# Kernel tuning notes

Hardware: AMD Instinct MI355X
Metric: run time of the kernel (lower is better)

The kernel has to match this reference:

```python
import jax, jax.numpy as jnp
import numpy as np

B, C, T = 16, 129, 2000
NF, ED, K = 40, 64, 16

def setup_inputs() -> dict:
    key = jax.random.key(0)
    ks = iter(jax.random.split(key, 48))
    def n(shape, s=0.05):
        return jax.random.normal(next(ks), shape, jnp.float32) * s
    inp = {
        'x': jax.random.normal(next(ks), (B, C, T), jnp.float32),
        # temporal conv (1,25) pad (0,12) + BN (inference running stats)
        'tconv_w': n((NF, 1, 1, 25)), 'tconv_b': jnp.zeros((NF,)),
        'tbn_g': jnp.ones((NF,)), 'tbn_b': jnp.zeros((NF,)), 'tbn_m': n((NF,)), 'tbn_v': jnp.ones((NF,)),
        # spatial conv (C,1) + BN
        'sconv_w': n((NF, NF, C, 1)), 'sconv_b': jnp.zeros((NF,)),
        'sbn_g': jnp.ones((NF,)), 'sbn_b': jnp.zeros((NF,)), 'sbn_m': n((NF,)), 'sbn_v': jnp.ones((NF,)),
        # separable: depthwise (1,15) pad (0,7), pointwise 1x1 -> 2*NF, BN
        'dw_w': n((NF, 1, 1, 15)), 'dw_b': jnp.zeros((NF,)),
        'pw_w': n((2 * NF, NF, 1, 1)), 'pw_b': jnp.zeros((2 * NF,)),
        'pbn_g': jnp.ones((2 * NF,)), 'pbn_b': jnp.zeros((2 * NF,)), 'pbn_m': n((2 * NF,)), 'pbn_v': jnp.ones((2 * NF,)),
        # projection 2*NF -> ED
        'proj_w': n((ED, 2 * NF)), 'proj_b': jnp.zeros((ED,)),
        # ENN cell 0 (input ED)
        'wx0': n((K, ED)), 'L0': jnp.eye(K, dtype=jnp.float32) + 0.1 * n((K, K), 1.0),
        'll0': jnp.asarray(np.log(0.1), jnp.float32), 'b0': jnp.zeros((K,)),
        'ln0_g': jnp.ones((K,)), 'ln0_b': jnp.zeros((K,)),
        # ENN cell 1 (input K)
        'wx1': n((K, K)), 'L1': jnp.eye(K, dtype=jnp.float32) + 0.1 * n((K, K), 1.0),
        'll1': jnp.asarray(np.log(0.1), jnp.float32), 'b1': jnp.zeros((K,)),
        'ln1_g': jnp.ones((K,)), 'ln1_b': jnp.zeros((K,)),
        # collapse
        'wq_w': n((K, K)), 'wq_b': jnp.zeros((K,)), 'log_temp': jnp.asarray(0.0, jnp.float32),
    }
    return inp

def _conv(x, w, b, pad, groups=1):
    y = jax.lax.conv_general_dilated(
        x, w, window_strides=(1, 1), padding=pad,
        dimension_numbers=('NCHW', 'OIHW', 'NCHW'), feature_group_count=groups)
    return y + b[None, :, None, None]

def _bn(x, g, b, m, v, eps=1e-5):
    inv = g / jnp.sqrt(v + eps)
    return x * inv[None, :, None, None] + (b - m * inv)[None, :, None, None]

def _cell(x, h, Wx, L, ll, b, g, be, eps=1e-5):
    E = L @ L.T  # PSD entanglement matrix [K,K]
    pre = x @ Wx.T + h @ E.T - jnp.exp(ll) * h + b
    mu = pre.mean(-1, keepdims=True)
    var = pre.var(-1, keepdims=True)
    pre = (pre - mu) / jnp.sqrt(var + eps) * g + be
    return jnp.tanh(pre)

def _forward(x, tconv_w, tconv_b, tbn_g, tbn_b, tbn_m, tbn_v,
             sconv_w, sconv_b, sbn_g, sbn_b, sbn_m, sbn_v,
             dw_w, dw_b, pw_w, pw_b, pbn_g, pbn_b, pbn_m, pbn_v,
             proj_w, proj_b,
             wx0, L0, ll0, b0, ln0_g, ln0_b,
             wx1, L1, ll1, b1, ln1_g, ln1_b,
             wq_w, wq_b, log_temp):
    # ---- SpatialCNN front-end (BN in inference mode, dropout=identity) ----
    o = x[:, None, :, :]                                        # [B,1,C,T]
    o = _conv(o, tconv_w, tconv_b, ((0, 0), (12, 12)))          # [B,NF,C,T]
    o = jax.nn.elu(_bn(o, tbn_g, tbn_b, tbn_m, tbn_v))
    o = _conv(o, sconv_w, sconv_b, ((0, 0), (0, 0)))            # [B,NF,1,T]
    o = jax.nn.elu(_bn(o, sbn_g, sbn_b, sbn_m, sbn_v))
    o = _conv(o, dw_w, dw_b, ((0, 0), (7, 7)), groups=NF)       # depthwise
    o = _conv(o, pw_w, pw_b, ((0, 0), (0, 0)))                  # [B,2NF,1,T]
    o = jax.nn.elu(_bn(o, pbn_g, pbn_b, pbn_m, pbn_v))
    Bn, Ch, _, Tt = o.shape
    o = o.reshape(Bn, Ch, Tt // 4, 4).mean(-1)                  # AvgPool (1,4) -> [B,2NF,T']
    feats = o.transpose(0, 2, 1) @ proj_w.T + proj_b            # [B,T',ED]
    # ---- Entangled RNN over T' steps (lax.scan) ----
    h_init = (jnp.zeros((Bn, K), feats.dtype), jnp.zeros((Bn, K), feats.dtype))
    def step(carry, xt):
        h0, h1 = carry
        h0 = _cell(xt, h0, wx0, L0, ll0, b0, ln0_g, ln0_b)
        h1 = _cell(h0, h1, wx1, L1, ll1, b1, ln1_g, ln1_b)
        return (h0, h1), None
    (h0, h1), _ = jax.lax.scan(step, h_init, feats.transpose(1, 0, 2))
    Z = h1                                                       # [B,K]
    # ---- Collapse attention ----
    q = Z @ wq_w.T + wq_b
    scores = jnp.sum(q * Z, axis=-1, keepdims=True)              # [B,1]
    alpha = jax.nn.softmax(scores / jnp.exp(log_temp), axis=-1)  # [B,1]
    return Z, alpha

def reference(x, tconv_w, tconv_b, tbn_g, tbn_b, tbn_m, tbn_v,
              sconv_w, sconv_b, sbn_g, sbn_b, sbn_m, sbn_v,
              dw_w, dw_b, pw_w, pw_b, pbn_g, pbn_b, pbn_m, pbn_v,
              proj_w, proj_b,
              wx0, L0, ll0, b0, ln0_g, ln0_b,
              wx1, L1, ll1, b1, ln1_g, ln1_b,
              wq_w, wq_b, log_temp):
    return _forward(x, tconv_w, tconv_b, tbn_g, tbn_b, tbn_m, tbn_v,
                    sconv_w, sconv_b, sbn_g, sbn_b, sbn_m, sbn_v,
                    dw_w, dw_b, pw_w, pw_b, pbn_g, pbn_b, pbn_m, pbn_v,
                    proj_w, proj_b,
                    wx0, L0, ll0, b0, ln0_g, ln0_b,
                    wx1, L1, ll1, b1, ln1_g, ln1_b,
                    wq_w, wq_b, log_temp)
```

## Files before the change

### kernel.cpp

```cpp
#include <hip/hip_runtime.h>
#include <math.h>

#define B_ 16
#define C_ 129
#define T_ 2000
#define NF_ 40
#define ED_ 64
#define K_ 16
#define TP_ 500

#define OFF_SB2 1040
#define OFF_PWC 1088
#define OFF_PB2 4288
#define OFF_WP  4368
#define OFF_BP  5648
#define OFF_M0  5664
#define OFF_M1  5920
#define OFF_W1A 6224
#define OFF_W2U 8192
#define OFF_XP  1495040
#define OFF_S2R 1623040

typedef __attribute__((ext_vector_type(8))) short s8v;
typedef __attribute__((ext_vector_type(4))) float f4v;

#define XROW 292

__device__ __forceinline__ float elu_f(float x) {
    return x > 0.f ? x : (__expf(x) - 1.f);
}
__device__ __forceinline__ float tanh2e_f(float a2) {
    return fmaf(-2.f,
                __builtin_amdgcn_rcpf(__builtin_amdgcn_exp2f(a2) + 1.f), 1.f);
}
__device__ __forceinline__ unsigned bfr(float v) {
    return (__float_as_uint(v) + 0x8000u) >> 16;
}

#define DPPF(v, ctrl) __int_as_float(__builtin_amdgcn_update_dpp( \
    0, __float_as_int(v), (ctrl), 0xF, 0xF, false))

#define RSUM16(s) do {                     \
    s += DPPF(s, 0x128);                   \
    s += DPPF(s, 0x124);                   \
    s += DPPF(s, 0x122);                   \
    s += DPPF(s, 0x121);                   \
} while (0)

#define RDLANE(v, L) __int_as_float(__builtin_amdgcn_readlane(__float_as_int(v), (L)))

#define C2F 2.8853900817779268f

struct P0 {
    const float *tconv_w, *tconv_b, *tbn_g, *tbn_b, *tbn_m, *tbn_v;
    const float *sconv_b, *sbn_g, *sbn_b, *sbn_m, *sbn_v;
    const float *pw_w, *pw_b, *pbn_g, *pbn_b, *pbn_m, *pbn_v;
    const float *proj_w, *proj_b, *wx0, *b0, *L0, *ll0, *L1, *ll1;
    const float *sconv_w;
    float* ws;
};

__global__ __launch_bounds__(256) void k0_all(P0 p) {
    const int tid = threadIdx.x;
    float* ws = p.ws;
    const float eps = 1e-5f;

    if (blockIdx.x < 1250) {
        const int i = blockIdx.x * 256 + tid;
        if (i < 320000)
            ((float4*)(ws + OFF_S2R))[i] = make_float4(0.f, 0.f, 0.f, 0.f);
        return;
    }
    if (blockIdx.x < 1444) {
        const int e = (blockIdx.x - 1250) * 256 + tid;
        if (e >= C_ * 3 * 2 * 64) return;
        unsigned short* w2b = (unsigned short*)(ws + OFF_W2U);
        const int c = e / 384;
        int r = e - c * 384;
        const int mt = r >> 7; r &= 127;
        const int kc = r >> 6;
        const int lane = r & 63;
        const int g = mt * 16 + (lane & 15);
        const float sinv = (g < NF_) ? p.sbn_g[g] * rsqrtf(p.sbn_v[g] + 1e-5f) : 0.f;
        unsigned short o[8];
#pragma unroll
        for (int j = 0; j < 8; ++j) {
            const int f = kc * 32 + (lane >> 4) * 8 + j;
            float v = 0.f;
            if (g < NF_ && f < NF_) v = p.sconv_w[g * (NF_ * C_) + f * C_ + c] * sinv;
            o[j] = (unsigned short)bfr(v);
        }
        unsigned short* dst = w2b + (size_t)e * 8;
#pragma unroll
        for (int j = 0; j < 8; ++j) dst[j] = o[j];
        return;
    }

    const int gtid = (blockIdx.x - 1444) * 256 + tid;
    const int stride = 8 * 256;
    for (int e = gtid; e < 192; e += stride) {
        const int mt = e >> 6, L = e & 63;
        const int f = mt * 16 + (L & 15);
        float inv = 0.f, bias = 0.f;
        if (f < NF_) {
            inv = p.tbn_g[f] / sqrtf(p.tbn_v[f] + eps);
            bias = p.tconv_b[f] * inv + p.tbn_b[f] - p.tbn_m[f] * inv;
        }
        unsigned short* dst = ((unsigned short*)(ws + OFF_W1A)) + e * 8;
#pragma unroll
        for (int j = 0; j < 8; ++j) {
            const int k = (L >> 4) * 8 + j;
            float v = 0.f;
            if (f < NF_) {
                if (k < 25) v = p.tconv_w[f * 25 + k] * inv;
                else if (k == 25) v = bias;
            }
            dst[j] = (unsigned short)bfr(v);
        }
    }
    for (int f = gtid; f < NF_; f += stride) {
        const float sinv = p.sbn_g[f] / sqrtf(p.sbn_v[f] + eps);
        ws[OFF_SB2 + f] = p.sconv_b[f] * sinv + p.sbn_b[f] - p.sbn_m[f] * sinv;
    }
    for (int e = gtid; e < 3200; e += stride) {
        const int g = e / 40;
        const float pinv = p.pbn_g[g] / sqrtf(p.pbn_v[g] + eps);
        ws[OFF_PWC + e] = p.pw_w[e] * pinv;
    }
    for (int g = gtid; g < 80; g += stride) {
        const float pinv = p.pbn_g[g] / sqrtf(p.pbn_v[g] + eps);
        ws[OFF_PB2 + g] = p.pw_b[g] * pinv + p.pbn_b[g] - p.pbn_m[g] * pinv;
    }
    for (int e = gtid; e < 1280; e += stride) {
        const int k = e / 80, g = e - k * 80;
        float a = 0.f;
        for (int ee = 0; ee < ED_; ++ee)
            a = fmaf(p.wx0[k * ED_ + ee], p.proj_w[ee * 80 + g], a);
        ws[OFF_WP + e] = a;
    }
    for (int k = gtid; k < K_; k += stride) {
        float a = p.b0[k];
        for (int ee = 0; ee < ED_; ++ee)
            a = fmaf(p.wx0[k * ED_ + ee], p.proj_b[ee], a);
        ws[OFF_BP + k] = a;
    }
    for (int e = gtid; e < 256; e += stride) {
        const int k = e >> 4, j = e & 15;
        float a0 = 0.f, a1 = 0.f;
        for (int i = 0; i < 16; ++i) {
            a0 = fmaf(p.L0[k * 16 + i], p.L0[j * 16 + i], a0);
            a1 = fmaf(p.L1[k * 16 + i], p.L1[j * 16 + i], a1);
        }
        if (k == j) { a0 -= expf(p.ll0[0]); a1 -= expf(p.ll1[0]); }
        ws[OFF_M0 + e] = a0;
        ws[OFF_M1 + e] = a1;
    }
}

__global__ __launch_bounds__(256, 4) void k1_mfma(
    const float* __restrict__ x, const unsigned short* __restrict__ w1a,
    const unsigned short* __restrict__ w2b, float* __restrict__ s2raw) {
    __shared__ float xs[17 * XROW];
    __shared__ unsigned int vsI[2048];

    const int tid = threadIdx.x;
    const int split = blockIdx.x & 7;
    const int tile = (blockIdx.x >> 3) & 7;
    const int b = blockIdx.x >> 6;
    const int c0 = (split * C_) >> 3;
    const int c1 = ((split + 1) * C_) >> 3;
    const int cc = c1 - c0;
    const int t0 = tile << 8;
    const int w = tid >> 6;
    const int lane = tid & 63;
    const int n = lane & 15;
    const int q = lane >> 4;
    const int qh = q >> 1;
    const int q1_2 = (q & 1) * 2;
    const bool q3 = (q == 3);
    const int wb = w << 9;
    const int w64 = w << 6;
    const int ln8 = n + q * 8;

    for (int i = tid; i < 2048; i += 256) vsI[i] = 0u;
    for (int e = tid; e < cc * XROW; e += 256) {
        const int cl = e / XROW;
        const int i = e - cl * XROW;
        const int t = t0 - 12 + i;
        float v = 0.f;
        if ((unsigned)t < (unsigned)T_) v = x[(b * C_ + c0 + cl) * T_ + t];
        xs[e] = v;
    }
    __syncthreads();

    const s8v* w1a8 = (const s8v*)w1a;
    s8v wA[3];
#pragma unroll
    for (int mt = 0; mt < 3; ++mt) wA[mt] = w1a8[mt * 64 + lane];

    f4v acc[4][3];
#pragma unroll
    for (int nt = 0; nt < 4; ++nt)
#pragma unroll
        for (int mt = 0; mt < 3; ++mt) acc[nt][mt] = (f4v)0.f;

    const s8v* w2b8 = (const s8v*)w2b;
    const f4v z4 = (f4v)0.f;

    for (int cl = 0; cl < cc; ++cl) {
        const int c = c0 + cl;
        s8v af[3][2];
#pragma unroll
        for (int mt = 0; mt < 3; ++mt)
#pragma unroll
            for (int kc = 0; kc < 2; ++kc)
                af[mt][kc] = w2b8[((c * 3 + mt) * 2 + kc) * 64 + lane];

        const float* xrow = &xs[cl * XROW + w64 + ln8];

#pragma unroll
        for (int nt = 0; nt < 4; ++nt) {
            float bx[8];
#pragma unroll
            for (int j = 0; j < 8; ++j) bx[j] = xrow[nt * 16 + j];
            if (q3) bx[1] = 1.0f;
            unsigned pw_[4];
#pragma unroll
            for (int jj = 0; jj < 4; ++jj)
                pw_[jj] = bfr(bx[2 * jj]) |
                    ((__float_as_uint(bx[2 * jj + 1]) + 0x8000u) & 0xFFFF0000u);
            const s8v bh = *(const s8v*)pw_;
#pragma unroll
            for (int mt = 0; mt < 3; ++mt) {
                const f4v vT = __builtin_amdgcn_mfma_f32_16x16x32_bf16(
                    wA[mt], bh, z4, 0, 0, 0);
                const float e0 = elu_f(vT[0]);
                const float e1 = elu_f(vT[1]);
                const float e2 = elu_f(vT[2]);
                const float e3 = elu_f(vT[3]);
                const unsigned lo = bfr(e0) |
                    ((__float_as_uint(e1) + 0x8000u) & 0xFFFF0000u);
                const unsigned hi = bfr(e2) |
                    ((__float_as_uint(e3) + 0x8000u) & 0xFFFF0000u);
                const int base = wb + ((2 * mt + qh) << 6) + (n << 2) + q1_2;
                vsI[base] = lo;
                vsI[base + 1] = hi;
            }
            __builtin_amdgcn_wave_barrier();
            const s8v b0 = *(const s8v*)&vsI[wb + (q << 6) + (n << 2)];
            const s8v b1 = *(const s8v*)&vsI[wb + ((4 + q) << 6) + (n << 2)];
#pragma unroll
            for (int mt = 0; mt < 3; ++mt) {
                acc[nt][mt] = __builtin_amdgcn_mfma_f32_16x16x32_bf16(
                    af[mt][0], b0, acc[nt][mt], 0, 0, 0);
                acc[nt][mt] = __builtin_amdgcn_mfma_f32_16x16x32_bf16(
                    af[mt][1], b1, acc[nt][mt], 0, 0, 0);
            }
            __builtin_amdgcn_wave_barrier();
        }
    }

#pragma unroll
    for (int nt = 0; nt < 4; ++nt) {
        const int t = t0 + w * 64 + nt * 16 + n;
        if (t >= T_) continue;
#pragma unroll
        for (int mt = 0; mt < 3; ++mt) {
#pragma unroll
            for (int r = 0; r < 4; ++r) {
                const int g = mt * 16 + q * 4 + r;
                if (g < NF_)
                    atomicAdd(&s2raw[(b * NF_ + g) * T_ + t], acc[nt][mt][r]);
            }
        }
    }
}

__global__ __launch_bounds__(256) void k2_dwpw(
    const float* __restrict__ s2raw, const float* __restrict__ sb2,
    const float* __restrict__ dw_w, const float* __restrict__ dw_b,
    const float* __restrict__ pwc, const float* __restrict__ pb2,
    const float* __restrict__ WP, const float* __restrict__ bp,
    float* __restrict__ xp) {
    __shared__ float st[NF_ * 114];
    __shared__ float dwo[NF_ * 100];
    __shared__ float dwwl[NF_ * 15];
    __shared__ float dwbl[NF_];
    __shared__ float pwcl[80 * 40];
    __shared__ float pb2l[80];
    __shared__ float WPl[K_ * 80];
    __shared__ float bpl[K_];
    __shared__ float po[80 * 25];
    const int tid = threadIdx.x;
    const int b = blockIdx.x / 20;
    const int tp0 = (blockIdx.x % 20) * 25;
    const int tbase = tp0 * 4 - 7;
    for (int e = tid; e < NF_ * 114; e += 256) {
        const int f = e / 114;
        const int i = e - f * 114;
        const int t = tbase + i;
        float v = 0.f;
        if ((unsigned)t < (unsigned)T_)
            v = elu_f(s2raw[(b * NF_ + f) * T_ + t] + sb2[f]);
        st[e] = v;
    }
    for (int e = tid; e < 600; e += 256) dwwl[e] = dw_w[e];
    for (int e = tid; e < 3200; e += 256) pwcl[e] = pwc[e];
    for (int e = tid; e < 1280; e += 256) WPl[e] = WP[e];
    if (tid < NF_) dwbl[tid] = dw_b[tid];
    if (tid < 80) pb2l[tid] = pb2[tid];
    if (tid < K_) bpl[tid] = bp[tid];
    __syncthreads();
    for (int e = tid; e < 4000; e += 256) {
        const int f = e / 100;
        const int tq = e - f * 100;
        float a = dwbl[f];
#pragma unroll
        for (int kk = 0; kk < 15; ++kk)
            a = fmaf(dwwl[f * 15 + kk], st[f * 114 + tq + kk], a);
        dwo[e] = a;
    }
    __syncthreads();
    for (int e = tid; e < 2000; e += 256) {
        const int g = e / 25;
        const int tp = e - g * 25;
        float sum = 0.f;
#pragma unroll
        for (int dt = 0; dt < 4; ++dt) {
            float a = pb2l[g];
            for (int f = 0; f < NF_; ++f)
                a = fmaf(pwcl[g * 40 + f], dwo[f * 100 + tp * 4 + dt], a);
            sum += elu_f(a);
        }
        po[e] = sum * 0.25f;
    }
    __syncthreads();
    for (int e = tid; e < 400; e += 256) {
        const int tp = e >> 4;
        const int k = e & 15;
        float a = bpl[k];
        for (int g = 0; g < 80; ++g)
            a = fmaf(WPl[k * 80 + g], po[g * 25 + tp], a);
        xp[(b * TP_ + tp0 + tp) * K_ + k] = a;
    }
}

#define SCAN_STEP(I, S) do {                                              \
    float sH0[16], sH1[16];                                               \
    _Pragma("unroll")                                                     \
    for (int j = 0; j < 16; ++j) {                                        \
        sH0[j] = RDLANE(vA, 32 + j);                                      \
        sH1[j] = RDLANE(vA, j);                                           \
    }                                                                     \
    float a0 = 0.f, a1 = 0.f, a2 = 0.f, a3 = 0.f;                         \
    float c0 = 0.f, c1 = 0.f, c2 = 0.f, c3 = 0.f;                         \
    _Pragma("unroll")                                                     \
    for (int j = 0; j < 16; j += 4) {                                     \
        a0 = fmaf(WA[j],     sH0[j],     a0);                             \
        a1 = fmaf(WA[j + 1], sH0[j + 1], a1);                             \
        a2 = fmaf(WA[j + 2], sH0[j + 2], a2);                             \
        a3 = fmaf(WA[j + 3], sH0[j + 3], a3);                             \
        c0 = fmaf(WB[j],     sH1[j],     c0);                             \
        c1 = fmaf(WB[j + 1], sH1[j + 1], c1);                             \
        c2 = fmaf(WB[j + 2], sH1[j + 2], c2);                             \
        c3 = fmaf(WB[j + 3], sH1[j + 3], c3);                             \
    }                                                                     \
    const float xv = xn[S];                                               \
    int tf = (I) + 5; if (tf > TP_ - 1) tf = TP_ - 1;                     \
    xn[S] = xpb[tf * K_];                                                 \
    const float cadd = lower ? b1r : xv;                                  \
    const float pre = (((a0 + a1) + (a2 + a3)) +                          \
                       ((c0 + c1) + (c2 + c3))) + cadd;                   \
    float s1 = pre, s2 = pre * pre;                                       \
    RSUM16(s1);                                                           \
    RSUM16(s2);                                                           \
    const float mu = s1 * 0.0625f;                                        \
    const float var = fmaf(s2, 0.0625f, -mu * mu);                        \
    vA = tanh2e_f(fmaf((pre - mu) * rsqrtf(var + 1e-5f), gg, bb));        \
} while (0)

__global__ __launch_bounds__(64, 1) void k3_scan(
    const float* __restrict__ xp, const float* __restrict__ M0,
    const float* __restrict__ M1, const float* __restrict__ wx1,
    const float* __restrict__ b1, const float* __restrict__ ln0_g,
    const float* __restrict__ ln0_b, const float* __restrict__ ln1_g,
    const float* __restrict__ ln1_b, float* __restrict__ out) {
    const int lane = threadIdx.x;
    const int k = lane & 15;
    const bool lower = lane < 32;
    const int b = blockIdx.x;

    float WA[16], WB[16];
#pragma unroll
    for (int j = 0; j < 16; ++j) {
        const float m0 = M0[k * 16 + j];
        const float m1 = M1[k * 16 + j];
        const float wx = wx1[k * 16 + j];
        WA[j] = lower ? wx : m0;
        WB[j] = lower ? m1 : 0.f;
    }
    const float b1r = b1[k];
    const float g0 = C2F * ln0_g[k], be0 = C2F * ln0_b[k];
    const float gg = lower ? C2F * ln1_g[k] : g0;
    const float bb = lower ? C2F * ln1_b[k] : be0;
    const float* xpb = xp + b * TP_ * K_ + k;

    float h0_0;
    {
        const float x0 = xpb[0];
        float s1 = x0, s2 = x0 * x0;
        RSUM16(s1);
        RSUM16(s2);
        const float mu = s1 * 0.0625f;
        const float var = fmaf(s2, 0.0625f, -mu * mu);
        h0_0 = tanh2e_f(fmaf((x0 - mu) * rsqrtf(var + 1e-5f), g0, be0));
    }
    float vA = lower ? 0.f : h0_0;

    float xn[4];
    xn[0] = xpb[1 * K_];
    xn[1] = xpb[2 * K_];
    xn[2] = xpb[3 * K_];
    xn[3] = xpb[4 * K_];

    for (int i = 0; i < TP_; i += 4) {
        SCAN_STEP(i + 0, 0);
        SCAN_STEP(i + 1, 1);
        SCAN_STEP(i + 2, 2);
        SCAN_STEP(i + 3, 3);
    }
    if (lane < 16) {
        out[b * K_ + k] = vA;
        if (k == 0) out[256 + b] = 1.0f;
    }
}

extern "C" void kernel_launch(void* const* d_in, const int* in_sizes, int n_in,
                              void* d_out, int out_size, void* d_ws, size_t ws_size,
                              hipStream_t stream) {
    const float* x       = (const float*)d_in[0];
    const float* dw_w    = (const float*)d_in[13];
    const float* dw_b    = (const float*)d_in[14];
    const float* wx1     = (const float*)d_in[29];
    const float* b1      = (const float*)d_in[32];
    const float* ln0_g   = (const float*)d_in[27];
    const float* ln0_b   = (const float*)d_in[28];
    const float* ln1_g   = (const float*)d_in[33];
    const float* ln1_b   = (const float*)d_in[34];
    float* ws = (float*)d_ws;
    float* out = (float*)d_out;

    P0 p;
    p.tconv_w = (const float*)d_in[1]; p.tconv_b = (const float*)d_in[2];
    p.tbn_g = (const float*)d_in[3]; p.tbn_b = (const float*)d_in[4];
    p.tbn_m = (const float*)d_in[5]; p.tbn_v = (const float*)d_in[6];
    p.sconv_b = (const float*)d_in[8];
    p.sbn_g = (const float*)d_in[9]; p.sbn_b = (const float*)d_in[10];
    p.sbn_m = (const float*)d_in[11]; p.sbn_v = (const float*)d_in[12];
    p.pw_w = (const float*)d_in[15]; p.pw_b = (const float*)d_in[16];
    p.pbn_g = (const float*)d_in[17]; p.pbn_b = (const float*)d_in[18];
    p.pbn_m = (const float*)d_in[19]; p.pbn_v = (const float*)d_in[20];
    p.proj_w = (const float*)d_in[21]; p.proj_b = (const float*)d_in[22];
    p.wx0 = (const float*)d_in[23]; p.b0 = (const float*)d_in[26];
    p.L0 = (const float*)d_in[24]; p.ll0 = (const float*)d_in[25];
    p.L1 = (const float*)d_in[30]; p.ll1 = (const float*)d_in[31];
    p.sconv_w = (const float*)d_in[7];
    p.ws = ws;

    unsigned short* w2b = (unsigned short*)(ws + OFF_W2U);
    unsigned short* w1a = (unsigned short*)(ws + OFF_W1A);

    k0_all<<<dim3(1452), dim3(256), 0, stream>>>(p);
    k1_mfma<<<dim3(1024), dim3(256), 0, stream>>>(x, w1a, w2b, ws + OFF_S2R);
    k2_dwpw<<<dim3(320), dim3(256), 0, stream>>>(ws + OFF_S2R, ws + OFF_SB2,
                                                 dw_w, dw_b, ws + OFF_PWC,
                                                 ws + OFF_PB2, ws + OFF_WP, ws + OFF_BP,
                                                 ws + OFF_XP);
    k3_scan<<<dim3(16), dim3(64), 0, stream>>>(ws + OFF_XP, ws + OFF_M0, ws + OFF_M1,
                                               wx1, b1, ln0_g, ln0_b, ln1_g, ln1_b, out);
}
```

Before: 369.8 us.

## Replace split-K atomic accumulation with per-split slices reduced in consumer kernel

Each of the eight channel splits in the spatial MFMA kernel now writes its partial sums to its own workspace slice with plain stores instead of atomicAdd into one buffer. The depthwise/pointwise kernel then sums the eight slices while loading. This removes atomic contention and the need to zero the accumulation buffer, at the cost of eight times the intermediate memory traffic in the reader. The path is enabled only when the workspace is large enough, so whether it runs depends on the harness workspace size.

```diff
diff --git a/kernel.cpp b/kernel.cpp
--- a/kernel.cpp
+++ b/kernel.cpp
@@ -20,6 +20,7 @@
 #define OFF_W2U 8192
 #define OFF_XP  1495040
 #define OFF_S2R 1623040
+#define SLICE_  1280000
 
 typedef __attribute__((ext_vector_type(8))) short s8v;
 typedef __attribute__((ext_vector_type(4))) float f4v;
@@ -159,7 +160,8 @@
 
 __global__ __launch_bounds__(256, 4) void k1_mfma(
     const float* __restrict__ x, const unsigned short* __restrict__ w1a,
-    const unsigned short* __restrict__ w2b, float* __restrict__ s2raw) {
+    const unsigned short* __restrict__ w2b, float* __restrict__ s2raw,
+    int multi) {
     __shared__ float xs[17 * XROW];
     __shared__ unsigned int vsI[2048];
 
@@ -260,17 +262,35 @@
         }
     }
 
-#pragma unroll
-    for (int nt = 0; nt < 4; ++nt) {
-        const int t = t0 + w * 64 + nt * 16 + n;
-        if (t >= T_) continue;
-#pragma unroll
-        for (int mt = 0; mt < 3; ++mt) {
-#pragma unroll
-            for (int r = 0; r < 4; ++r) {
-                const int g = mt * 16 + q * 4 + r;
-                if (g < NF_)
-                    atomicAdd(&s2raw[(b * NF_ + g) * T_ + t], acc[nt][mt][r]);
+    if (multi) {
+        float* dst = s2raw + (size_t)split * SLICE_;
+#pragma unroll
+        for (int nt = 0; nt < 4; ++nt) {
+            const int t = t0 + w * 64 + nt * 16 + n;
+            if (t >= T_) continue;
+#pragma unroll
+            for (int mt = 0; mt < 3; ++mt) {
+#pragma unroll
+                for (int r = 0; r < 4; ++r) {
+                    const int g = mt * 16 + q * 4 + r;
+                    if (g < NF_)
+                        dst[(b * NF_ + g) * T_ + t] = acc[nt][mt][r];
+                }
+            }
+        }
+    } else {
+#pragma unroll
+        for (int nt = 0; nt < 4; ++nt) {
+            const int t = t0 + w * 64 + nt * 16 + n;
+            if (t >= T_) continue;
+#pragma unroll
+            for (int mt = 0; mt < 3; ++mt) {
+#pragma unroll
+                for (int r = 0; r < 4; ++r) {
+                    const int g = mt * 16 + q * 4 + r;
+                    if (g < NF_)
+                        atomicAdd(&s2raw[(b * NF_ + g) * T_ + t], acc[nt][mt][r]);
+                }
             }
         }
     }
@@ -281,7 +301,7 @@
     const float* __restrict__ dw_w, const float* __restrict__ dw_b,
     const float* __restrict__ pwc, const float* __restrict__ pb2,
     const float* __restrict__ WP, const float* __restrict__ bp,
-    float* __restrict__ xp) {
+    float* __restrict__ xp, int multi) {
     __shared__ float st[NF_ * 114];
     __shared__ float dwo[NF_ * 100];
     __shared__ float dwwl[NF_ * 15];
@@ -300,8 +320,20 @@
         const int i = e - f * 114;
         const int t = tbase + i;
         float v = 0.f;
-        if ((unsigned)t < (unsigned)T_)
-            v = elu_f(s2raw[(b * NF_ + f) * T_ + t] + sb2[f]);
+        if ((unsigned)t < (unsigned)T_) {
+            const float* p0 = s2raw + (b * NF_ + f) * T_ + t;
+            float s;
+            if (multi) {
+                const float s01 = p0[0] + p0[SLICE_];
+                const float s23 = p0[2 * SLICE_] + p0[3 * SLICE_];
+                const float s45 = p0[4 * SLICE_] + p0[5 * SLICE_];
+                const float s67 = p0[6 * SLICE_] + p0[7 * SLICE_];
+                s = (s01 + s23) + (s45 + s67);
+            } else {
+                s = p0[0];
+            }
+            v = elu_f(s + sb2[f]);
+        }
         st[e] = v;
     }
     for (int e = tid; e < 600; e += 256) dwwl[e] = dw_w[e];
@@ -470,12 +502,16 @@
     unsigned short* w2b = (unsigned short*)(ws + OFF_W2U);
     unsigned short* w1a = (unsigned short*)(ws + OFF_W1A);
 
+    const int multi =
+        (ws_size >= (size_t)(OFF_S2R + 8 * SLICE_) * sizeof(float)) ? 1 : 0;
+
     k0_all<<<dim3(1452), dim3(256), 0, stream>>>(p);
-    k1_mfma<<<dim3(1024), dim3(256), 0, stream>>>(x, w1a, w2b, ws + OFF_S2R);
+    k1_mfma<<<dim3(1024), dim3(256), 0, stream>>>(x, w1a, w2b, ws + OFF_S2R,
+                                                  multi);
     k2_dwpw<<<dim3(320), dim3(256), 0, stream>>>(ws + OFF_S2R, ws + OFF_SB2,
                                                  dw_w, dw_b, ws + OFF_PWC,
                                                  ws + OFF_PB2, ws + OFF_WP, ws + OFF_BP,
-                                                 ws + OFF_XP);
+                                                 ws + OFF_XP, multi);
     k3_scan<<<dim3(16), dim3(64), 0, stream>>>(ws + OFF_XP, ws + OFF_M0, ws + OFF_M1,
                                                wx1, b1, ln0_g, ln0_b, ln1_g, ln1_b, out);
 }
```

After: 361.0 us. -2.4%, faster.
